# Kernel optimization log

Measured on AMD Instinct MI355X. Metric: run time of the kernel, lower is better.

The kernel has to match this reference:

```python
import jax, jax.numpy as jnp
import numpy as np

N_HEADS = 16

def setup_inputs() -> dict:
    key = jax.random.key(0)
    ks = jax.random.split(key, 7)
    B, T, C = 2, 2048, 1024
    s = 0.02  # weight init scale
    return {
        "x": jax.random.normal(ks[0], (B, T, C), jnp.float32),
        "attention_mask": jnp.ones((B, T), jnp.float32),
        "Wq": jax.random.normal(ks[1], (C, C), jnp.float32) * s,
        "Wk": jax.random.normal(ks[2], (C, C), jnp.float32) * s,
        "Wv": jax.random.normal(ks[3], (C, C), jnp.float32) * s,
        "Wp": jax.random.normal(ks[4], (C, C), jnp.float32) * s,
        "bp": jax.random.normal(ks[5], (C,), jnp.float32) * s,
    }

def reference(x, attention_mask, Wq, Wk, Wv, Wp, bp):
    B, T, C = x.shape
    H = N_HEADS
    d = C // H
    q = (x @ Wq).reshape(B, T, H, d)
    k = (x @ Wk).reshape(B, T, H, d)
    v = (x @ Wv).reshape(B, T, H, d)
    # scores scaled by C**-0.5 (embedding dim), as in the source
    wei = jnp.einsum('bihd,bjhd->bhij', q, k) * (C ** -0.5)
    causal = jnp.tril(jnp.ones((T, T), bool))  # tril buffer, T == block_size
    wei = jnp.where(causal[None, None], wei, -jnp.inf)
    wei = jax.nn.softmax(wei, axis=-1)
    # NOTE: source's post-softmax padding masked_fill is not in-place -> no-op.
    # Dropout in eval mode -> identity.
    out = jnp.einsum('bhij,bjhd->bihd', wei, v).reshape(B, T, C)
    return out @ Wp + bp
```

## Files before the change

kernel.cpp:

```cpp
#include <hip/hip_runtime.h>
#include <hip/hip_bf16.h>
#include <stdint.h>

#define BB 2
#define TT 2048
#define CC 1024
#define HH 16
#define DD 64
#define MM (BB*TT)

#define C2SCALE 0.045084220027780106f

typedef __bf16 bf16x8 __attribute__((ext_vector_type(8)));
typedef float f32x4 __attribute__((ext_vector_type(4)));

__device__ __forceinline__ void load_lds16(const void* g, void* l) {
    __builtin_amdgcn_global_load_lds((const __attribute__((address_space(1))) uint32_t*)g,
                                     (__attribute__((address_space(3))) uint32_t*)l,
                                     16, 0, 0);
}

__global__ __launch_bounds__(256)
void conv_bf16(const float* __restrict__ in, __hip_bfloat16* __restrict__ out, int n4) {
    int i = blockIdx.x * 256 + threadIdx.x;
    if (i >= n4) return;
    float4 f = reinterpret_cast<const float4*>(in)[i];
    union { __hip_bfloat16 h[4]; uint2 u; } cv;
    cv.h[0] = __float2bfloat16(f.x);
    cv.h[1] = __float2bfloat16(f.y);
    cv.h[2] = __float2bfloat16(f.z);
    cv.h[3] = __float2bfloat16(f.w);
    reinterpret_cast<uint2*>(out)[i] = cv.u;
}

__global__ __launch_bounds__(256)
void transpose_conv(const float* __restrict__ W, __hip_bfloat16* __restrict__ Wt) {
    __shared__ float t[32][33];
    int kt = blockIdx.x * 32, nt = blockIdx.y * 32;
    int tx = threadIdx.x & 31, ty = threadIdx.x >> 5;
#pragma unroll
    for (int r = 0; r < 32; r += 8)
        t[ty + r][tx] = W[(size_t)(kt + ty + r) * CC + nt + tx];
    __syncthreads();
#pragma unroll
    for (int r = 0; r < 32; r += 8)
        Wt[(size_t)(nt + ty + r) * CC + kt + tx] = __float2bfloat16(t[tx][ty + r]);
}

template <int MODE>
__global__ __launch_bounds__(256)
void gemm_bt(const __hip_bfloat16* __restrict__ A,
             const __hip_bfloat16* __restrict__ Bt,
             void* __restrict__ out0, void* __restrict__ out1, void* __restrict__ out2,
             const float* __restrict__ bias,
             int M, int N, int K) {
    __shared__ __hip_bfloat16 As[128 * 64];
    __shared__ __hip_bfloat16 Bs[128 * 64];

    const int tid = threadIdx.x;
    const int wave = tid >> 6, lane = tid & 63;
    const int lg = lane >> 4, lr = lane & 15;
    const int wm = wave >> 1, wn = wave & 1;
    const int bm0 = blockIdx.y * 128, bn0 = blockIdx.x * 128;

    f32x4 acc[4][4] = {};

    for (int k0 = 0; k0 < K; k0 += 64) {
        __syncthreads();
#pragma unroll
        for (int it = 0; it < 4; ++it) {
            int c = it * 256 + tid;
            int row = c >> 3, sub = c & 7;
            int g = sub ^ (row & 7);
            load_lds16((const char*)(A + (size_t)(bm0 + row) * K + k0) + g * 16,
                       (char*)As + c * 16);
        }
#pragma unroll
        for (int it = 0; it < 4; ++it) {
            int c = it * 256 + tid;
            int row = c >> 3, sub = c & 7;
            int g = sub ^ (row & 7);
            load_lds16((const char*)(Bt + (size_t)(bn0 + row) * K + k0) + g * 16,
                       (char*)Bs + c * 16);
        }
        __syncthreads();

        bf16x8 af[2][4], bf[2][4];
#pragma unroll
        for (int kk = 0; kk < 2; ++kk) {
#pragma unroll
            for (int m = 0; m < 4; ++m) {
                int row = wm * 64 + m * 16 + lr;
                af[kk][m] = *(const bf16x8*)((const char*)As + row * 128 + (((kk * 4 + lg) ^ (row & 7)) * 16));
            }
#pragma unroll
            for (int n = 0; n < 4; ++n) {
                int row = wn * 64 + n * 16 + lr;
                bf[kk][n] = *(const bf16x8*)((const char*)Bs + row * 128 + (((kk * 4 + lg) ^ (row & 7)) * 16));
            }
        }
#pragma unroll
        for (int kk = 0; kk < 2; ++kk)
#pragma unroll
            for (int m = 0; m < 4; ++m)
#pragma unroll
                for (int n = 0; n < 4; ++n)
                    acc[m][n] = __builtin_amdgcn_mfma_f32_16x16x32_bf16(af[kk][m], bf[kk][n], acc[m][n], 0, 0, 0);
    }

#pragma unroll
    for (int m = 0; m < 4; ++m)
#pragma unroll
        for (int n = 0; n < 4; ++n) {
            int row0 = bm0 + wm * 64 + m * 16 + lg * 4;
            int colf = bn0 + wn * 64 + n * 16 + lr;
            if (MODE == 2) {
#pragma unroll
                for (int r = 0; r < 4; ++r)
                    ((float*)out0)[(size_t)(row0 + r) * N + colf] = acc[m][n][r] + bias[colf];
            } else {
                int which = colf >> 10, col = colf & 1023;
                if (which < 2) {
                    __hip_bfloat16* o = which ? (__hip_bfloat16*)out1 : (__hip_bfloat16*)out0;
                    float sc = which ? 1.0f : C2SCALE;
#pragma unroll
                    for (int r = 0; r < 4; ++r)
                        o[(size_t)(row0 + r) * 1024 + col] = __float2bfloat16(acc[m][n][r] * sc);
                } else {
                    int hh = col >> 6, dd = col & 63;
                    int bI = row0 >> 11, tt = row0 & 2047;
                    union { __hip_bfloat16 h[4]; uint2 u; } pk;
#pragma unroll
                    for (int r = 0; r < 4; ++r) pk.h[r] = __float2bfloat16(acc[m][n][r]);
                    *(uint2*)((__hip_bfloat16*)out2 + ((size_t)(bI * HH + hh) * DD + dd) * TT + tt) = pk.u;
                }
            }
        }
}

__global__ __launch_bounds__(256)
void attn_kernel(const __hip_bfloat16* __restrict__ Q,
                 const __hip_bfloat16* __restrict__ K,
                 const __hip_bfloat16* __restrict__ Vt,
                 __hip_bfloat16* __restrict__ att) {
    __shared__ __hip_bfloat16 Ks[2][64 * 64];
    __shared__ __hip_bfloat16 Vs[2][64 * 64];
    __shared__ __hip_bfloat16 Pl[4][32 * 72];

    const int tid = threadIdx.x;
    const int wave = tid >> 6, lane = tid & 63;
    const int lg = lane >> 4, lr = lane & 15;

    int id = blockIdx.x;
    int rest = id >> 3;
    int qt = rest & 15;
    int hb = (id & 7) + ((rest >> 4) << 3);
    const int h = hb & 15, b = hb >> 4;
    if (b & 1) qt = 15 - qt;

    const size_t baseQK = ((size_t)b * TT) * CC + (size_t)h * DD;
    const __hip_bfloat16* Vth = Vt + ((size_t)(b * HH + h)) * DD * TT;
    const int wq0 = qt * 128 + wave * 32;

    bf16x8 qf[2][2];
#pragma unroll
    for (int mf = 0; mf < 2; ++mf)
#pragma unroll
        for (int kf = 0; kf < 2; ++kf)
            qf[mf][kf] = *(const bf16x8*)&Q[baseQK + (size_t)(wq0 + mf * 16 + lr) * CC + kf * 32 + lg * 8];

    float m_run[2], l_run[2];
    f32x4 o[2][4] = {};
#pragma unroll
    for (int mf = 0; mf < 2; ++mf) { m_run[mf] = -1e30f; l_run[mf] = 0.f; }

    const int nkt = qt * 2 + 2;

    auto stage = [&](int bufi, int kv0) {
#pragma unroll
        for (int it = 0; it < 2; ++it) {
            int c = it * 256 + tid;
            int row = c >> 3, sub = c & 7;
            int g = sub ^ (row & 7);
            load_lds16((const char*)(K + baseQK + (size_t)(kv0 + row) * CC) + g * 16,
                       (char*)Ks[bufi] + c * 16);
            load_lds16((const char*)(Vth + (size_t)row * TT + kv0) + g * 16,
                       (char*)Vs[bufi] + c * 16);
        }
    };

    stage(0, 0);

    for (int kt = 0; kt < nkt; ++kt) {
        const int kv0 = kt * 64;
        __syncthreads();
        if (kt + 1 < nkt) stage((kt + 1) & 1, kv0 + 64);
        const char* Kb = (const char*)Ks[kt & 1];
        const char* Vb = (const char*)Vs[kt & 1];

        if (kv0 > wq0 + 31) continue;

        f32x4 s[2][4] = {};
#pragma unroll
        for (int kf = 0; kf < 2; ++kf) {
            bf16x8 kfr[4];
#pragma unroll
            for (int nf = 0; nf < 4; ++nf)
                kfr[nf] = *(const bf16x8*)(Kb + (nf * 16 + lr) * 128 + (((kf * 4 + lg) ^ (lr & 7)) * 16));
#pragma unroll
            for (int mf = 0; mf < 2; ++mf)
#pragma unroll
                for (int nf = 0; nf < 4; ++nf)
                    s[mf][nf] = __builtin_amdgcn_mfma_f32_16x16x32_bf16(kfr[nf], qf[mf][kf], s[mf][nf], 0, 0, 0);
        }

        const bool needMask = (kv0 + 63 > wq0);
#pragma unroll
        for (int mf = 0; mf < 2; ++mf) {
            const int qg = wq0 + mf * 16 + lr;
            float mx = -1e30f;
#pragma unroll
            for (int nf = 0; nf < 4; ++nf)
#pragma unroll
                for (int r = 0; r < 4; ++r) {
                    float sv = s[mf][nf][r];
                    if (needMask) {
                        int kvg = kv0 + nf * 16 + lg * 4 + r;
                        sv = (kvg > qg) ? -1e30f : sv;
                        s[mf][nf][r] = sv;
                    }
                    mx = fmaxf(mx, sv);
                }
            mx = fmaxf(mx, __shfl_xor(mx, 16, 64));
            mx = fmaxf(mx, __shfl_xor(mx, 32, 64));
            float mold = m_run[mf];
            float mnew = fmaxf(mold, mx);
            float sc = __builtin_amdgcn_exp2f(mold - mnew);
            float rsum = 0.f;
#pragma unroll
            for (int nf = 0; nf < 4; ++nf)
#pragma unroll
                for (int r = 0; r < 4; ++r) {
                    float p = __builtin_amdgcn_exp2f(s[mf][nf][r] - mnew);
                    s[mf][nf][r] = p;
                    rsum += p;
                }
            rsum += __shfl_xor(rsum, 16, 64);
            rsum += __shfl_xor(rsum, 32, 64);
            l_run[mf] = l_run[mf] * sc + rsum;
            m_run[mf] = mnew;
#pragma unroll
            for (int r = 0; r < 4; ++r) {
                float sco = __shfl(sc, lg * 4 + r, 64);
#pragma unroll
                for (int df = 0; df < 4; ++df) o[mf][df][r] *= sco;
            }
        }

        __hip_bfloat16* Pw = &Pl[wave][0];
#pragma unroll
        for (int mf = 0; mf < 2; ++mf)
#pragma unroll
            for (int nf = 0; nf < 4; ++nf)
#pragma unroll
                for (int r = 0; r < 4; ++r)
                    Pw[(mf * 16 + lr) * 72 + nf * 16 + lg * 4 + r] = __float2bfloat16(s[mf][nf][r]);

#pragma unroll
        for (int ks = 0; ks < 2; ++ks) {
            bf16x8 pf[2], vf[4];
#pragma unroll
            for (int mf = 0; mf < 2; ++mf)
                pf[mf] = *(const bf16x8*)&Pw[(mf * 16 + lr) * 72 + ks * 32 + lg * 8];
#pragma unroll
            for (int df = 0; df < 4; ++df)
                vf[df] = *(const bf16x8*)(Vb + (df * 16 + lr) * 128 + (((ks * 4 + lg) ^ (lr & 7)) * 16));
#pragma unroll
            for (int mf = 0; mf < 2; ++mf)
#pragma unroll
                for (int df = 0; df < 4; ++df)
                    o[mf][df] = __builtin_amdgcn_mfma_f32_16x16x32_bf16(pf[mf], vf[df], o[mf][df], 0, 0, 0);
        }
    }

#pragma unroll
    for (int mf = 0; mf < 2; ++mf)
#pragma unroll
        for (int r = 0; r < 4; ++r) {
            float lo = __shfl(l_run[mf], lg * 4 + r, 64);
            float inv = 1.0f / lo;
            int qg = wq0 + mf * 16 + lg * 4 + r;
#pragma unroll
            for (int df = 0; df < 4; ++df)
                att[baseQK + (size_t)qg * CC + df * 16 + lr] = __float2bfloat16(o[mf][df][r] * inv);
        }
}

extern "C" void kernel_launch(void* const* d_in, const int* in_sizes, int n_in,
                              void* d_out, int out_size, void* d_ws, size_t ws_size,
                              hipStream_t stream) {
    const float* x  = (const float*)d_in[0];
    const float* Wq = (const float*)d_in[2];
    const float* Wk = (const float*)d_in[3];
    const float* Wv = (const float*)d_in[4];
    const float* Wp = (const float*)d_in[5];
    const float* bp = (const float*)d_in[6];
    float* out = (float*)d_out;

    __hip_bfloat16* ws  = (__hip_bfloat16*)d_ws;
    __hip_bfloat16* xb  = ws;
    __hip_bfloat16* wqt = xb  + (size_t)MM * CC;
    __hip_bfloat16* wkt = wqt + (size_t)CC * CC;
    __hip_bfloat16* wvt = wkt + (size_t)CC * CC;
    __hip_bfloat16* wpt = wvt + (size_t)CC * CC;
    __hip_bfloat16* Qb  = wpt + (size_t)CC * CC;
    __hip_bfloat16* Kb  = Qb  + (size_t)MM * CC;
    __hip_bfloat16* VtG = Kb  + (size_t)MM * CC;
    __hip_bfloat16* att = VtG + (size_t)MM * CC;

    conv_bf16<<<(MM * CC / 4 + 255) / 256, 256, 0, stream>>>(x, xb, MM * CC / 4);
    dim3 tg(CC / 32, CC / 32);
    transpose_conv<<<tg, 256, 0, stream>>>(Wq, wqt);
    transpose_conv<<<tg, 256, 0, stream>>>(Wk, wkt);
    transpose_conv<<<tg, 256, 0, stream>>>(Wv, wvt);
    transpose_conv<<<tg, 256, 0, stream>>>(Wp, wpt);

    dim3 gq(3 * CC / 128, MM / 128);
    gemm_bt<1><<<gq, 256, 0, stream>>>(xb, wqt, Qb, Kb, VtG, nullptr, MM, 3 * CC, CC);

    attn_kernel<<<dim3(512), 256, 0, stream>>>(Qb, Kb, VtG, att);

    dim3 gp(CC / 128, MM / 128);
    gemm_bt<2><<<gp, 256, 0, stream>>>(att, wpt, out, nullptr, nullptr, bp, MM, CC, CC);
}
```

Before: 215.1 us.

## Use 8 waves per attention block, lazy softmax rescale, and batch weight transposes

The attention kernel now runs 512 threads per block, each wave owning 16 query rows instead of 32. This cuts per-wave register use and causal tail work, and one K/V staging pass now covers all threads. Online softmax skips rescaling the output accumulator unless the row max grows by more than a threshold (8 in log2 units). P tiles are written to LDS with packed 64-bit stores. The four weight transpose launches are merged into one 3D-grid launch. Each K/V tile loaded into LDS is now reused by fewer query rows per wave, and the lazy rescale lets unnormalized exponentials reach up to about 2^8 before rescaling.

```diff
diff --git a/kernel.cpp b/kernel.cpp
--- a/kernel.cpp
+++ b/kernel.cpp
@@ -34,8 +34,13 @@
 }
 
 __global__ __launch_bounds__(256)
-void transpose_conv(const float* __restrict__ W, __hip_bfloat16* __restrict__ Wt) {
+void transpose_conv4(const float* __restrict__ W0, const float* __restrict__ W1,
+                     const float* __restrict__ W2, const float* __restrict__ W3,
+                     __hip_bfloat16* __restrict__ out) {
     __shared__ float t[32][33];
+    const int z = blockIdx.z;
+    const float* W = (z == 0) ? W0 : (z == 1) ? W1 : (z == 2) ? W2 : W3;
+    __hip_bfloat16* Wt = out + (size_t)z * CC * CC;
     int kt = blockIdx.x * 32, nt = blockIdx.y * 32;
     int tx = threadIdx.x & 31, ty = threadIdx.x >> 5;
 #pragma unroll
@@ -138,14 +143,14 @@
         }
 }
 
-__global__ __launch_bounds__(256)
+__global__ __launch_bounds__(512)
 void attn_kernel(const __hip_bfloat16* __restrict__ Q,
                  const __hip_bfloat16* __restrict__ K,
                  const __hip_bfloat16* __restrict__ Vt,
                  __hip_bfloat16* __restrict__ att) {
     __shared__ __hip_bfloat16 Ks[2][64 * 64];
     __shared__ __hip_bfloat16 Vs[2][64 * 64];
-    __shared__ __hip_bfloat16 Pl[4][32 * 72];
+    __shared__ __hip_bfloat16 Pl[8][16 * 72];
 
     const int tid = threadIdx.x;
     const int wave = tid >> 6, lane = tid & 63;
@@ -160,33 +165,25 @@
 
     const size_t baseQK = ((size_t)b * TT) * CC + (size_t)h * DD;
     const __hip_bfloat16* Vth = Vt + ((size_t)(b * HH + h)) * DD * TT;
-    const int wq0 = qt * 128 + wave * 32;
-
-    bf16x8 qf[2][2];
-#pragma unroll
-    for (int mf = 0; mf < 2; ++mf)
-#pragma unroll
-        for (int kf = 0; kf < 2; ++kf)
-            qf[mf][kf] = *(const bf16x8*)&Q[baseQK + (size_t)(wq0 + mf * 16 + lr) * CC + kf * 32 + lg * 8];
-
-    float m_run[2], l_run[2];
-    f32x4 o[2][4] = {};
-#pragma unroll
-    for (int mf = 0; mf < 2; ++mf) { m_run[mf] = -1e30f; l_run[mf] = 0.f; }
+    const int wq0 = qt * 128 + wave * 16;
+
+    bf16x8 qf[2];
+#pragma unroll
+    for (int kf = 0; kf < 2; ++kf)
+        qf[kf] = *(const bf16x8*)&Q[baseQK + (size_t)(wq0 + lr) * CC + kf * 32 + lg * 8];
+
+    float m_run = -1e30f, l_run = 0.f;
+    f32x4 o[4] = {};
 
     const int nkt = qt * 2 + 2;
 
     auto stage = [&](int bufi, int kv0) {
-#pragma unroll
-        for (int it = 0; it < 2; ++it) {
-            int c = it * 256 + tid;
-            int row = c >> 3, sub = c & 7;
-            int g = sub ^ (row & 7);
-            load_lds16((const char*)(K + baseQK + (size_t)(kv0 + row) * CC) + g * 16,
-                       (char*)Ks[bufi] + c * 16);
-            load_lds16((const char*)(Vth + (size_t)row * TT + kv0) + g * 16,
-                       (char*)Vs[bufi] + c * 16);
-        }
+        int row = tid >> 3, sub = tid & 7;
+        int g = sub ^ (row & 7);
+        load_lds16((const char*)(K + baseQK + (size_t)(kv0 + row) * CC) + g * 16,
+                   (char*)Ks[bufi] + tid * 16);
+        load_lds16((const char*)(Vth + (size_t)row * TT + kv0) + g * 16,
+                   (char*)Vs[bufi] + tid * 16);
     };
 
     stage(0, 0);
@@ -198,9 +195,9 @@
         const char* Kb = (const char*)Ks[kt & 1];
         const char* Vb = (const char*)Vs[kt & 1];
 
-        if (kv0 > wq0 + 31) continue;
-
-        f32x4 s[2][4] = {};
+        if (kv0 > wq0 + 15) continue;
+
+        f32x4 s[4] = {};
 #pragma unroll
         for (int kf = 0; kf < 2; ++kf) {
             bf16x8 kfr[4];
@@ -208,92 +205,89 @@
             for (int nf = 0; nf < 4; ++nf)
                 kfr[nf] = *(const bf16x8*)(Kb + (nf * 16 + lr) * 128 + (((kf * 4 + lg) ^ (lr & 7)) * 16));
 #pragma unroll
-            for (int mf = 0; mf < 2; ++mf)
-#pragma unroll
-                for (int nf = 0; nf < 4; ++nf)
-                    s[mf][nf] = __builtin_amdgcn_mfma_f32_16x16x32_bf16(kfr[nf], qf[mf][kf], s[mf][nf], 0, 0, 0);
+            for (int nf = 0; nf < 4; ++nf)
+                s[nf] = __builtin_amdgcn_mfma_f32_16x16x32_bf16(kfr[nf], qf[kf], s[nf], 0, 0, 0);
         }
 
         const bool needMask = (kv0 + 63 > wq0);
-#pragma unroll
-        for (int mf = 0; mf < 2; ++mf) {
-            const int qg = wq0 + mf * 16 + lr;
-            float mx = -1e30f;
-#pragma unroll
-            for (int nf = 0; nf < 4; ++nf)
-#pragma unroll
-                for (int r = 0; r < 4; ++r) {
-                    float sv = s[mf][nf][r];
-                    if (needMask) {
-                        int kvg = kv0 + nf * 16 + lg * 4 + r;
-                        sv = (kvg > qg) ? -1e30f : sv;
-                        s[mf][nf][r] = sv;
-                    }
-                    mx = fmaxf(mx, sv);
+        const int qg = wq0 + lr;
+        float mx = -1e30f;
+#pragma unroll
+        for (int nf = 0; nf < 4; ++nf)
+#pragma unroll
+            for (int r = 0; r < 4; ++r) {
+                float sv = s[nf][r];
+                if (needMask) {
+                    int kvg = kv0 + nf * 16 + lg * 4 + r;
+                    sv = (kvg > qg) ? -1e30f : sv;
+                    s[nf][r] = sv;
                 }
-            mx = fmaxf(mx, __shfl_xor(mx, 16, 64));
-            mx = fmaxf(mx, __shfl_xor(mx, 32, 64));
-            float mold = m_run[mf];
-            float mnew = fmaxf(mold, mx);
-            float sc = __builtin_amdgcn_exp2f(mold - mnew);
-            float rsum = 0.f;
-#pragma unroll
-            for (int nf = 0; nf < 4; ++nf)
-#pragma unroll
-                for (int r = 0; r < 4; ++r) {
-                    float p = __builtin_amdgcn_exp2f(s[mf][nf][r] - mnew);
-                    s[mf][nf][r] = p;
-                    rsum += p;
-                }
-            rsum += __shfl_xor(rsum, 16, 64);
-            rsum += __shfl_xor(rsum, 32, 64);
-            l_run[mf] = l_run[mf] * sc + rsum;
-            m_run[mf] = mnew;
+                mx = fmaxf(mx, sv);
+            }
+        mx = fmaxf(mx, __shfl_xor(mx, 16, 64));
+        mx = fmaxf(mx, __shfl_xor(mx, 32, 64));
+
+        bool grow = __any(mx > m_run + 8.0f);
+        float sc = 0.0f;
+        if (grow) {
+            float mnew = fmaxf(m_run, mx);
+            sc = __builtin_amdgcn_exp2f(m_run - mnew);
+            m_run = mnew;
+        }
+        float rsum = 0.f;
+#pragma unroll
+        for (int nf = 0; nf < 4; ++nf)
+#pragma unroll
+            for (int r = 0; r < 4; ++r) {
+                float p = __builtin_amdgcn_exp2f(s[nf][r] - m_run);
+                s[nf][r] = p;
+                rsum += p;
+            }
+        rsum += __shfl_xor(rsum, 16, 64);
+        rsum += __shfl_xor(rsum, 32, 64);
+        if (grow) {
+            l_run = l_run * sc + rsum;
 #pragma unroll
             for (int r = 0; r < 4; ++r) {
                 float sco = __shfl(sc, lg * 4 + r, 64);
 #pragma unroll
-                for (int df = 0; df < 4; ++df) o[mf][df][r] *= sco;
-            }
+                for (int df = 0; df < 4; ++df) o[df][r] *= sco;
+            }
+        } else {
+            l_run += rsum;
         }
 
         __hip_bfloat16* Pw = &Pl[wave][0];
 #pragma unroll
-        for (int mf = 0; mf < 2; ++mf)
-#pragma unroll
-            for (int nf = 0; nf < 4; ++nf)
-#pragma unroll
-                for (int r = 0; r < 4; ++r)
-                    Pw[(mf * 16 + lr) * 72 + nf * 16 + lg * 4 + r] = __float2bfloat16(s[mf][nf][r]);
+        for (int nf = 0; nf < 4; ++nf) {
+            union { __hip_bfloat16 h[4]; uint2 u; } pk;
+#pragma unroll
+            for (int r = 0; r < 4; ++r) pk.h[r] = __float2bfloat16(s[nf][r]);
+            *(uint2*)&Pw[lr * 72 + nf * 16 + lg * 4] = pk.u;
+        }
 
 #pragma unroll
         for (int ks = 0; ks < 2; ++ks) {
-            bf16x8 pf[2], vf[4];
-#pragma unroll
-            for (int mf = 0; mf < 2; ++mf)
-                pf[mf] = *(const bf16x8*)&Pw[(mf * 16 + lr) * 72 + ks * 32 + lg * 8];
+            bf16x8 pf = *(const bf16x8*)&Pw[lr * 72 + ks * 32 + lg * 8];
+            bf16x8 vf[4];
 #pragma unroll
             for (int df = 0; df < 4; ++df)
                 vf[df] = *(const bf16x8*)(Vb + (df * 16 + lr) * 128 + (((ks * 4 + lg) ^ (lr & 7)) * 16));
 #pragma unroll
-            for (int mf = 0; mf < 2; ++mf)
-#pragma unroll
-                for (int df = 0; df < 4; ++df)
-                    o[mf][df] = __builtin_amdgcn_mfma_f32_16x16x32_bf16(pf[mf], vf[df], o[mf][df], 0, 0, 0);
+            for (int df = 0; df < 4; ++df)
+                o[df] = __builtin_amdgcn_mfma_f32_16x16x32_bf16(pf, vf[df], o[df], 0, 0, 0);
         }
     }
 
 #pragma unroll
-    for (int mf = 0; mf < 2; ++mf)
-#pragma unroll
-        for (int r = 0; r < 4; ++r) {
-            float lo = __shfl(l_run[mf], lg * 4 + r, 64);
-            float inv = 1.0f / lo;
-            int qg = wq0 + mf * 16 + lg * 4 + r;
-#pragma unroll
-            for (int df = 0; df < 4; ++df)
-                att[baseQK + (size_t)qg * CC + df * 16 + lr] = __float2bfloat16(o[mf][df][r] * inv);
-        }
+    for (int r = 0; r < 4; ++r) {
+        float lo = __shfl(l_run, lg * 4 + r, 64);
+        float inv = 1.0f / lo;
+        int qg = wq0 + lg * 4 + r;
+#pragma unroll
+        for (int df = 0; df < 4; ++df)
+            att[baseQK + (size_t)qg * CC + df * 16 + lr] = __float2bfloat16(o[df][r] * inv);
+    }
 }
 
 extern "C" void kernel_launch(void* const* d_in, const int* in_sizes, int n_in,
@@ -310,25 +304,19 @@
     __hip_bfloat16* ws  = (__hip_bfloat16*)d_ws;
     __hip_bfloat16* xb  = ws;
     __hip_bfloat16* wqt = xb  + (size_t)MM * CC;
-    __hip_bfloat16* wkt = wqt + (size_t)CC * CC;
-    __hip_bfloat16* wvt = wkt + (size_t)CC * CC;
-    __hip_bfloat16* wpt = wvt + (size_t)CC * CC;
+    __hip_bfloat16* wpt = wqt + 3 * (size_t)CC * CC;
     __hip_bfloat16* Qb  = wpt + (size_t)CC * CC;
     __hip_bfloat16* Kb  = Qb  + (size_t)MM * CC;
     __hip_bfloat16* VtG = Kb  + (size_t)MM * CC;
     __hip_bfloat16* att = VtG + (size_t)MM * CC;
 
     conv_bf16<<<(MM * CC / 4 + 255) / 256, 256, 0, stream>>>(x, xb, MM * CC / 4);
-    dim3 tg(CC / 32, CC / 32);
-    transpose_conv<<<tg, 256, 0, stream>>>(Wq, wqt);
-    transpose_conv<<<tg, 256, 0, stream>>>(Wk, wkt);
-    transpose_conv<<<tg, 256, 0, stream>>>(Wv, wvt);
-    transpose_conv<<<tg, 256, 0, stream>>>(Wp, wpt);
+    transpose_conv4<<<dim3(CC / 32, CC / 32, 4), 256, 0, stream>>>(Wq, Wk, Wv, Wp, wqt);
 
     dim3 gq(3 * CC / 128, MM / 128);
     gemm_bt<1><<<gq, 256, 0, stream>>>(xb, wqt, Qb, Kb, VtG, nullptr, MM, 3 * CC, CC);
 
-    attn_kernel<<<dim3(512), 256, 0, stream>>>(Qb, Kb, VtG, att);
+    attn_kernel<<<dim3(512), 512, 0, stream>>>(Qb, Kb, VtG, att);
 
     dim3 gp(CC / 128, MM / 128);
     gemm_bt<2><<<gp, 256, 0, stream>>>(att, wpt, out, nullptr, nullptr, bp, MM, CC, CC);
```

Result: faster. 193.1 us (-10.2%).
